# Kernel optimization log

Measured on AMD Instinct MI355X. Metric: run time of the kernel, lower is better.

Reference implementation:

```python
import jax, jax.numpy as jnp
import numpy as np

B, S, D, H = 2, 2048, 1024, 16
DK = D // H


def setup_inputs() -> dict:
    key = jax.random.key(0)
    ks = jax.random.split(key, 12)
    sc = 1.0 / np.sqrt(D)
    return {
        "q": jax.random.normal(ks[0], (B, S, D), jnp.float32),
        "k": jax.random.normal(ks[1], (B, S, D), jnp.float32),
        "v": jax.random.normal(ks[2], (B, S, D), jnp.float32),
        "mask": jax.random.randint(ks[3], (B, S), 0, 2, jnp.int32),
        "Wq": jax.random.normal(ks[4], (D, D), jnp.float32) * sc,
        "bq": jnp.zeros((D,), jnp.float32),
        "Wk": jax.random.normal(ks[5], (D, D), jnp.float32) * sc,
        "bk": jnp.zeros((D,), jnp.float32),
        "Wv": jax.random.normal(ks[6], (D, D), jnp.float32) * sc,
        "bv": jnp.zeros((D,), jnp.float32),
        "Wo": jax.random.normal(ks[7], (D, D), jnp.float32) * sc,
        "bo": jnp.zeros((D,), jnp.float32),
    }


def reference(q, k, v, mask, Wq, bq, Wk, bk, Wv, bv, Wo, bo):
    # Projections (flax nn.Dense: x @ W + b)
    query = q @ Wq + bq          # [B,S,D]
    key_ = k @ Wk + bk
    value = v @ Wv + bv
    # split heads -> [B,H,S,DK]
    def split(x):
        return x.reshape(B, S, H, DK).transpose(0, 2, 1, 3)
    qh, kh, vh = split(query), split(key_), split(value)
    scores = jnp.einsum('bhqd,bhkd->bhqk', qh, kh) / jnp.sqrt(jnp.float32(DK))
    # Faithful to source: mask=(mask==0); where(mask==0, -1e10, scores)
    # i.e. positions where ORIGINAL mask != 0 are set to -1e10.
    m = (mask == 0)[:, None, None, :]          # [B,1,1,S] bool
    scores = jnp.where(~m, jnp.float32(-1e10), scores)
    attn = jax.nn.softmax(scores, axis=-1)     # dropout deterministic (eval)
    x = jnp.einsum('bhqk,bhkd->bhqd', attn, vh)
    x = x.transpose(0, 2, 1, 3).reshape(B, S, D)
    return x @ Wo + bo
```

## Files before the change

### kernel.cpp

```cpp
#include <hip/hip_runtime.h>
#include <hip/hip_bf16.h>

typedef unsigned short u16;
typedef unsigned int u32;
typedef __attribute__((ext_vector_type(8))) __bf16 bf16x8;
typedef __attribute__((ext_vector_type(4))) float f32x4;
typedef __attribute__((ext_vector_type(16))) float f32x16;

constexpr int Bz = 2, Sq = 2048, Dm = 1024, Hn = 16, DK = 64;

__device__ __forceinline__ u16 f2bf(float f) {
    u32 u = __builtin_bit_cast(u32, f);
    return (u16)((u + 0x7FFFu + ((u >> 16) & 1u)) >> 16);
}

__device__ __forceinline__ u32 pack_bf16(float a, float b) {
#if __has_builtin(__builtin_amdgcn_cvt_pk_bf16_f32)
    return __builtin_bit_cast(u32, __builtin_amdgcn_cvt_pk_bf16_f32(a, b));
#else
    return (u32)f2bf(a) | ((u32)f2bf(b) << 16);
#endif
}

__device__ __forceinline__ bf16x8 lds_frag(const u16* p) {
    return __builtin_bit_cast(bf16x8, *(const uint4*)p);
}
__device__ __forceinline__ bf16x8 gfrag(const u16* p) {
    return __builtin_bit_cast(bf16x8, *(const uint4*)p);
}
__device__ __forceinline__ int swz(int r) { return (r ^ (r >> 3)) & 7; }

__device__ __forceinline__ void gll16(const u16* g, u16* l) {
    __builtin_amdgcn_global_load_lds(
        (const __attribute__((address_space(1))) void*)g,
        (__attribute__((address_space(3))) void*)l, 16, 0, 0);
}

__global__ __launch_bounds__(256) void mha_prep(
    const float* __restrict__ q, const float* __restrict__ k,
    const float* __restrict__ v,
    const float* __restrict__ w0, const float* __restrict__ w1,
    const float* __restrict__ w2, const float* __restrict__ w3,
    const int* __restrict__ mask,
    u16* __restrict__ qkv_dst, u16* __restrict__ wt_dst,
    float* __restrict__ biasg, int* __restrict__ compg, int* __restrict__ nkg)
{
    __shared__ float tl[64 * 65];
    __shared__ int sc[256];
    const int z = blockIdx.z, tid = threadIdx.x;
    if (z < 3) {
        const float* s = (z == 0) ? q : (z == 1) ? k : v;
        u16* d = qkv_dst + (size_t)z * 4 * 1024 * 1024;
        size_t i = ((size_t)blockIdx.x * 256 + tid) * 8;
        float4 a = *(const float4*)(s + i);
        float4 b = *(const float4*)(s + i + 4);
        *(uint4*)(d + i) = make_uint4(pack_bf16(a.x, a.y), pack_bf16(a.z, a.w),
                                      pack_bf16(b.x, b.y), pack_bf16(b.z, b.w));
        return;
    }
    const int bx = blockIdx.x;
    if (bx >= 1026) return;
    if (bx >= 1024) {
        const int b = bx - 1024;
        const int* mp = mask + b * Sq;
        int4 m0_ = ((const int4*)mp)[tid * 2];
        int4 m1_ = ((const int4*)mp)[tid * 2 + 1];
        int a[8];
        a[0] = (m0_.x == 0); a[1] = (m0_.y == 0); a[2] = (m0_.z == 0); a[3] = (m0_.w == 0);
        a[4] = (m1_.x == 0); a[5] = (m1_.y == 0); a[6] = (m1_.z == 0); a[7] = (m1_.w == 0);
        int cnt = 0;
#pragma unroll
        for (int j = 0; j < 8; j++) cnt += a[j];
        sc[tid] = cnt;
        __syncthreads();
        for (int off = 1; off < 256; off <<= 1) {
            int u = (tid >= off) ? sc[tid - off] : 0;
            int vv = sc[tid];
            __syncthreads();
            sc[tid] = vv + u;
            __syncthreads();
        }
        const int incl = sc[tid];
        const int nk = sc[255];
        int pa = incl - cnt;
        int pi = nk + tid * 8 - pa;
        int* cp = compg + b * Sq;
        float* bbp = biasg + b * Sq;
#pragma unroll
        for (int j = 0; j < 8; j++) {
            int pos = a[j] ? pa++ : pi++;
            cp[tid * 8 + j] = pos;
            bbp[pos] = a[j] ? 0.f : -1.44269504e10f;
        }
        if (tid == 0) nkg[b] = nk;
        return;
    }
    const int zi = bx >> 8, t = bx & 255, tr = t >> 4, tc = t & 15;
    const float* src = (zi == 0) ? w0 : (zi == 1) ? w1 : (zi == 2) ? w2 : w3;
    u16* d = wt_dst + (size_t)zi * Dm * Dm;
    {
        int r = tid >> 2, cq = (tid & 3) * 16;
        const float* sp = src + (size_t)(tr * 64 + r) * Dm + tc * 64 + cq;
#pragma unroll
        for (int j = 0; j < 4; j++) {
            float4 vv = *(const float4*)(sp + j * 4);
            tl[r * 65 + cq + j * 4 + 0] = vv.x;
            tl[r * 65 + cq + j * 4 + 1] = vv.y;
            tl[r * 65 + cq + j * 4 + 2] = vv.z;
            tl[r * 65 + cq + j * 4 + 3] = vv.w;
        }
    }
    __syncthreads();
    {
        int rr = tid >> 2, cc = (tid & 3) * 16;
        u16* dp = d + (size_t)(tc * 64 + rr) * Dm + tr * 64 + cc;
        u32 px[8];
#pragma unroll
        for (int j = 0; j < 8; j++)
            px[j] = pack_bf16(tl[(cc + 2 * j) * 65 + rr], tl[(cc + 2 * j + 1) * 65 + rr]);
        *(uint4*)dp       = make_uint4(px[0], px[1], px[2], px[3]);
        *(uint4*)(dp + 8) = make_uint4(px[4], px[5], px[6], px[7]);
    }
}

__device__ __forceinline__ void gemm_core_128128(
    const u16* __restrict__ Ab, const u16* __restrict__ Bb,
    u16* As, u16* Bs, f32x4 (&acc)[4][4])
{
    const int tid = threadIdx.x, lane = tid & 63;
    const int wm = (tid >> 7) & 1, wn = (tid >> 6) & 1;
    const int frow = lane & 15, quad = lane >> 4;

#pragma unroll
    for (int mi = 0; mi < 4; mi++)
#pragma unroll
        for (int ni = 0; ni < 4; ni++) acc[mi][ni] = (f32x4){0.f, 0.f, 0.f, 0.f};

    for (int k0 = 0; k0 < 1024; k0 += 64) {
#pragma unroll
        for (int i = 0; i < 4; i++) {
            int id = tid + i * 256, r = id >> 3, c = id & 7;
            gll16(Ab + (size_t)r * 1024 + k0 + (c ^ swz(r)) * 8, As + (size_t)id * 8);
        }
#pragma unroll
        for (int i = 0; i < 4; i++) {
            int id = tid + i * 256, r = id >> 3, c = id & 7;
            gll16(Bb + (size_t)r * 1024 + k0 + (c ^ swz(r)) * 8, Bs + (size_t)id * 8);
        }
        __syncthreads();
#pragma unroll
        for (int ks = 0; ks < 2; ks++) {
            bf16x8 af[4], bfr[4];
#pragma unroll
            for (int mi = 0; mi < 4; mi++) {
                int r = wm * 64 + mi * 16 + frow;
                af[mi] = lds_frag(As + r * 64 + ((ks * 4 + quad) ^ swz(r)) * 8);
            }
#pragma unroll
            for (int ni = 0; ni < 4; ni++) {
                int r = wn * 64 + ni * 16 + frow;
                bfr[ni] = lds_frag(Bs + r * 64 + ((ks * 4 + quad) ^ swz(r)) * 8);
            }
#pragma unroll
            for (int mi = 0; mi < 4; mi++)
#pragma unroll
                for (int ni = 0; ni < 4; ni++)
                    acc[mi][ni] = __builtin_amdgcn_mfma_f32_16x16x32_bf16(
                        af[mi], bfr[ni], acc[mi][ni], 0, 0, 0);
        }
        __syncthreads();
    }
}

__device__ __forceinline__ void gemm_core_12864(
    const u16* __restrict__ Ab, const u16* __restrict__ Bb,
    u16* As, u16* Bs, f32x4 (&acc)[4][2])
{
    const int tid = threadIdx.x, lane = tid & 63;
    const int wm = (tid >> 7) & 1, wn = (tid >> 6) & 1;
    const int frow = lane & 15, quad = lane >> 4;

#pragma unroll
    for (int mi = 0; mi < 4; mi++)
#pragma unroll
        for (int ni = 0; ni < 2; ni++) acc[mi][ni] = (f32x4){0.f, 0.f, 0.f, 0.f};

    for (int k0 = 0; k0 < 1024; k0 += 64) {
#pragma unroll
        for (int i = 0; i < 4; i++) {
            int id = tid + i * 256, r = id >> 3, c = id & 7;
            gll16(Ab + (size_t)r * 1024 + k0 + (c ^ swz(r)) * 8, As + (size_t)id * 8);
        }
#pragma unroll
        for (int i = 0; i < 2; i++) {
            int id = tid + i * 256, r = id >> 3, c = id & 7;
            gll16(Bb + (size_t)r * 1024 + k0 + (c ^ swz(r)) * 8, Bs + (size_t)id * 8);
        }
        __syncthreads();
#pragma unroll
        for (int ks = 0; ks < 2; ks++) {
            bf16x8 af[4], bfr[2];
#pragma unroll
            for (int mi = 0; mi < 4; mi++) {
                int r = wm * 64 + mi * 16 + frow;
                af[mi] = lds_frag(As + r * 64 + ((ks * 4 + quad) ^ swz(r)) * 8);
            }
#pragma unroll
            for (int ni = 0; ni < 2; ni++) {
                int r = wn * 32 + ni * 16 + frow;
                bfr[ni] = lds_frag(Bs + r * 64 + ((ks * 4 + quad) ^ swz(r)) * 8);
            }
#pragma unroll
            for (int mi = 0; mi < 4; mi++)
#pragma unroll
                for (int ni = 0; ni < 2; ni++)
                    acc[mi][ni] = __builtin_amdgcn_mfma_f32_16x16x32_bf16(
                        af[mi], bfr[ni], acc[mi][ni], 0, 0, 0);
        }
        __syncthreads();
    }
}

__global__ __launch_bounds__(256, 3) void mha_proj_qkv(
    const u16* __restrict__ Qb, const u16* __restrict__ Kb, const u16* __restrict__ Vb,
    const u16* __restrict__ Wqt, const u16* __restrict__ Wkt, const u16* __restrict__ Wvt,
    const float* __restrict__ bq, const float* __restrict__ bk, const float* __restrict__ bv,
    const int* __restrict__ comp,
    u16* __restrict__ Qh, u16* __restrict__ Kh, u16* __restrict__ Vt)
{
    __shared__ __align__(16) u16 As[128 * 64];
    __shared__ __align__(16) u16 Bs[128 * 64];
    const int z = blockIdx.z, bx = blockIdx.x;
    const u16* Ab; const u16* Bb; const float* bias;
    int m0, n0;
    if (z < 2) {
        m0 = (bx & 31) * 128;
        n0 = (bx >> 5) * 128;
        Ab = ((z == 0) ? Qb : Kb) + (size_t)m0 * Dm;
        Bb = ((z == 0) ? Wqt : Wkt) + (size_t)n0 * Dm;
        bias = (z == 0) ? bq : bk;
    } else {
        m0 = (bx >> 5) * 128;
        n0 = (bx & 31) * 128;
        Ab = Wvt + (size_t)m0 * Dm;
        Bb = Vb + (size_t)n0 * Dm;
        bias = bv;
    }

    f32x4 acc[4][4];
    gemm_core_128128(Ab, Bb, As, Bs, acc);

    const int tid = threadIdx.x, lane = tid & 63;
    const int wm = (tid >> 7) & 1, wn = (tid >> 6) & 1;
    const int frow = lane & 15, quad = lane >> 4;
    u16* dstq = (z == 0) ? Qh : Kh;
#pragma unroll
    for (int mi = 0; mi < 4; mi++)
#pragma unroll
        for (int ni = 0; ni < 4; ni++)
#pragma unroll
            for (int r = 0; r < 4; r++) {
                int i = m0 + wm * 64 + mi * 16 + quad * 4 + r;
                int j = n0 + wn * 64 + ni * 16 + frow;
                if (z < 2) {
                    float val = acc[mi][ni][r] + bias[j];
                    int b = i >> 11, s = i & (Sq - 1);
                    int h = j >> 6, dk = j & (DK - 1);
                    int srow = (z == 1) ? comp[b * Sq + s] : s;
                    dstq[((size_t)(b * Hn + h) * Sq + srow) * DK + dk] = f2bf(val);
                } else {
                    float val = acc[mi][ni][r] + bias[i];
                    int h = i >> 6, dk = i & (DK - 1);
                    int bj = j >> 11, s = j & (Sq - 1);
                    int cs = comp[bj * Sq + s];
                    int sp = (cs & ~12) | ((cs & 4) << 1) | ((cs & 8) >> 1);
                    Vt[((size_t)(bj * Hn + h) * DK + dk) * Sq + sp] = f2bf(val);
                }
            }
}

__global__ __launch_bounds__(512, 4) void mha_attn(
    const u16* __restrict__ Qh, const u16* __restrict__ Kh, const u16* __restrict__ Vt,
    const float* __restrict__ biasg, const int* __restrict__ nkg,
    u16* __restrict__ X)
{
    const int bh = blockIdx.x;
    const int b = bh >> 4;
    const int q0 = blockIdx.y * 64;
    const int tid = threadIdx.x, lane = tid & 63, w = tid >> 6;
    const int wq = w & 1, p = w >> 1;
    const int qc = lane & 31, half = lane >> 5;
    constexpr float C2 = 0.125f * 1.44269504f;

    __shared__ __align__(16) u16 SB[128 * 64 + 64 * 128];
    __shared__ float lsl[256];
    u16* Ks = SB;
    u16* Vs = SB + 128 * 64;

    const u16* Qp = Qh + (size_t)bh * Sq * DK;
    const u16* Kp = Kh + (size_t)bh * Sq * DK;
    const u16* Vp = Vt + (size_t)bh * DK * Sq;
    const float* bp = biasg + b * Sq;
    const int nk = nkg[b];
    const int nt = (nk + 127) >> 7;

    bf16x8 qf[4];
    {
        const u16* qrow = Qp + (size_t)(q0 + wq * 32 + qc) * DK + half * 8;
#pragma unroll
        for (int kc = 0; kc < 4; kc++) qf[kc] = gfrag(qrow + kc * 16);
    }

    const int idA = tid, idB = tid + 512;
    const u16* ksA = Kp + (size_t)(idA >> 3) * DK + ((idA & 7) ^ swz(idA >> 3)) * 8;
    const u16* ksB = Kp + (size_t)(idB >> 3) * DK + ((idB & 7) ^ swz(idB >> 3)) * 8;
    const u16* vsA = Vp + (size_t)(idA >> 4) * Sq + (((idA & 15) ^ ((idA >> 4) & 15)) * 8);
    const u16* vsB = Vp + (size_t)(idB >> 4) * Sq + (((idB & 15) ^ ((idB >> 4) & 15)) * 8);
    u16* kdA = Ks + idA * 8;
    u16* kdB = Ks + idB * 8;
    u16* vdA = Vs + idA * 8;
    u16* vdB = Vs + idB * 8;

    auto stage = [&](int kb) {
        gll16(ksA + (size_t)kb * DK, kdA);
        gll16(ksB + (size_t)kb * DK, kdB);
        gll16(vsA + kb, vdA);
        gll16(vsB + kb, vdB);
    };

    const int kr = p * 32 + qc;
    int kfo[4];
#pragma unroll
    for (int kc = 0; kc < 4; kc++)
        kfo[kc] = kr * 64 + (((kc * 2 + half) ^ swz(kr)) * 8);
    int vfo0[2], vfo1[2];
#pragma unroll
    for (int kc = 0; kc < 2; kc++) {
        int ch = p * 4 + kc * 2 + half;
        vfo0[kc] = qc * 128 + ((ch ^ (qc & 15)) * 8);
        vfo1[kc] = (32 + qc) * 128 + ((ch ^ (qc & 15)) * 8);
    }
    const float* bpw = bp + p * 32 + 4 * half;

    float l_l = 0.f;
    f32x16 o0, o1;
#pragma unroll
    for (int i = 0; i < 16; i++) { o0[i] = 0.f; o1[i] = 0.f; }

    for (int it = 0; it < nt; it++) {
        stage(it * 128);
        __syncthreads();

        f32x16 sT;
#pragma unroll
        for (int i = 0; i < 16; i++) sT[i] = 0.f;
        __builtin_amdgcn_s_setprio(1);
#pragma unroll
        for (int kc = 0; kc < 4; kc++) {
            bf16x8 ka = lds_frag(Ks + kfo[kc]);
            sT = __builtin_amdgcn_mfma_f32_32x32x16_bf16(ka, qf[kc], sT, 0, 0, 0);
        }
        __builtin_amdgcn_s_setprio(0);

        const int kb = it * 128;
        float t[16], rs = 0.f;
#pragma unroll
        for (int g = 0; g < 4; g++) {
            float4 mb = *(const float4*)(bpw + kb + 8 * g);
#pragma unroll
            for (int r = 0; r < 4; r++) {
                float bb = (r == 0) ? mb.x : (r == 1) ? mb.y : (r == 2) ? mb.z : mb.w;
                float a = __builtin_amdgcn_exp2f(fmaf(sT[g * 4 + r], C2, bb));
                t[g * 4 + r] = a; rs += a;
            }
        }
        l_l += rs;

        u32 pk[8];
#pragma unroll
        for (int i = 0; i < 8; i++) pk[i] = pack_bf16(t[2 * i], t[2 * i + 1]);

        __builtin_amdgcn_s_setprio(1);
#pragma unroll
        for (int kc = 0; kc < 2; kc++) {
            bf16x8 pf = __builtin_bit_cast(bf16x8,
                make_uint4(pk[4 * kc], pk[4 * kc + 1], pk[4 * kc + 2], pk[4 * kc + 3]));
            bf16x8 va0 = lds_frag(Vs + vfo0[kc]);
            bf16x8 va1 = lds_frag(Vs + vfo1[kc]);
            o0 = __builtin_amdgcn_mfma_f32_32x32x16_bf16(va0, pf, o0, 0, 0, 0);
            o1 = __builtin_amdgcn_mfma_f32_32x32x16_bf16(va1, pf, o1, 0, 0, 0);
        }
        __builtin_amdgcn_s_setprio(0);
        __syncthreads();
    }

    l_l += __shfl_xor(l_l, 32);
    float* fcb = (float*)SB;
    if (p >= 2) {
        float* fc = fcb + (size_t)(wq * 2 + (p & 1)) * 2048;
#pragma unroll
        for (int r = 0; r < 16; r++) fc[r * 64 + lane] = o0[r];
#pragma unroll
        for (int r = 0; r < 16; r++) fc[(16 + r) * 64 + lane] = o1[r];
        lsl[(wq * 2 + (p & 1)) * 64 + lane] = l_l;
    }
    __syncthreads();
    if (p < 2) {
        float* fc = fcb + (size_t)(wq * 2 + p) * 2048;
#pragma unroll
        for (int r = 0; r < 16; r++) o0[r] += fc[r * 64 + lane];
#pragma unroll
        for (int r = 0; r < 16; r++) o1[r] += fc[(16 + r) * 64 + lane];
        l_l += lsl[(wq * 2 + p) * 64 + lane];
    }
    if (p == 1) {
        float* fc = fcb + (size_t)(wq * 2 + 1) * 2048;
#pragma unroll
        for (int r = 0; r < 16; r++) fc[r * 64 + lane] = o0[r];
#pragma unroll
        for (int r = 0; r < 16; r++) fc[(16 + r) * 64 + lane] = o1[r];
        lsl[(wq * 2 + 1) * 64 + lane] = l_l;
    }
    __syncthreads();
    if (p == 0) {
        float* fc = fcb + (size_t)(wq * 2 + 1) * 2048;
#pragma unroll
        for (int r = 0; r < 16; r++) o0[r] += fc[r * 64 + lane];
#pragma unroll
        for (int r = 0; r < 16; r++) o1[r] += fc[(16 + r) * 64 + lane];
        l_l += lsl[(wq * 2 + 1) * 64 + lane];
        float inv = 1.0f / l_l;
        const int qg = q0 + wq * 32 + qc;
        u16* Xp = X + (size_t)(b * Sq + qg) * Dm + (bh & 15) * DK;
#pragma unroll
        for (int g = 0; g < 4; g++) {
            *(uint2*)&Xp[8 * g + 4 * half] =
                make_uint2(pack_bf16(o0[g * 4 + 0] * inv, o0[g * 4 + 1] * inv),
                           pack_bf16(o0[g * 4 + 2] * inv, o0[g * 4 + 3] * inv));
            *(uint2*)&Xp[32 + 8 * g + 4 * half] =
                make_uint2(pack_bf16(o1[g * 4 + 0] * inv, o1[g * 4 + 1] * inv),
                           pack_bf16(o1[g * 4 + 2] * inv, o1[g * 4 + 3] * inv));
        }
    }
}

__global__ __launch_bounds__(256) void mha_oproj(
    const u16* __restrict__ X, const u16* __restrict__ Wot,
    const float* __restrict__ bo, float* __restrict__ out)
{
    __shared__ __align__(16) u16 As[128 * 64];
    __shared__ __align__(16) u16 Bs[64 * 64];
    const int bx = blockIdx.x;
    const int m0 = (bx & 31) * 128, n0 = (bx >> 5) * 64;
    f32x4 acc[4][2];
    gemm_core_12864(X + (size_t)m0 * Dm, Wot + (size_t)n0 * Dm, As, Bs, acc);
    const int tid = threadIdx.x, lane = tid & 63;
    const int wm = (tid >> 7) & 1, wn = (tid >> 6) & 1;
    const int frow = lane & 15, quad = lane >> 4;
#pragma unroll
    for (int mi = 0; mi < 4; mi++)
#pragma unroll
        for (int ni = 0; ni < 2; ni++)
#pragma unroll
            for (int r = 0; r < 4; r++) {
                int m = m0 + wm * 64 + mi * 16 + quad * 4 + r;
                int n = n0 + wn * 32 + ni * 16 + frow;
                out[(size_t)m * Dm + n] = acc[mi][ni][r] + bo[n];
            }
}

extern "C" void kernel_launch(void* const* d_in, const int* in_sizes, int n_in,
                              void* d_out, int out_size, void* d_ws, size_t ws_size,
                              hipStream_t stream)
{
    const float* qin  = (const float*)d_in[0];
    const float* kin  = (const float*)d_in[1];
    const float* vin  = (const float*)d_in[2];
    const int*   mask = (const int*)d_in[3];
    const float* Wq   = (const float*)d_in[4];
    const float* bq   = (const float*)d_in[5];
    const float* Wk   = (const float*)d_in[6];
    const float* bk   = (const float*)d_in[7];
    const float* Wv   = (const float*)d_in[8];
    const float* bv   = (const float*)d_in[9];
    const float* Wo   = (const float*)d_in[10];
    const float* bo   = (const float*)d_in[11];
    float* out = (float*)d_out;

    u16* ws = (u16*)d_ws;
    const size_t MW = (size_t)Dm * Dm;
    const size_t MT = (size_t)Bz * Sq * Dm;
    u16* Wqt = ws;
    u16* Wkt = ws + MW;
    u16* Wvt = ws + 2 * MW;
    u16* Wot = ws + 3 * MW;
    u16* Qb  = ws + 4 * MW;
    u16* Kb  = Qb + MT;
    u16* Vb  = Kb + MT;
    u16* Qh  = Vb + MT;
    u16* Kh  = Qh + MT;
    u16* Vt  = Kh + MT;
    float* biasg = (float*)(Vt + MT);
    int*   compg = (int*)(biasg + Bz * Sq);
    int*   nkg   = (int*)(compg + Bz * Sq);
    u16* X   = Qb;

    hipLaunchKernelGGL(mha_prep, dim3(2048, 1, 4), dim3(256), 0, stream,
                       qin, kin, vin, Wq, Wk, Wv, Wo, mask, Qb, Wqt, biasg, compg, nkg);
    hipLaunchKernelGGL(mha_proj_qkv, dim3(256, 1, 3), dim3(256), 0, stream,
                       Qb, Kb, Vb, Wqt, Wkt, Wvt, bq, bk, bv, compg, Qh, Kh, Vt);
    hipLaunchKernelGGL(mha_attn, dim3(32, 32), dim3(512), 0, stream,
                       Qh, Kh, Vt, biasg, nkg, X);
    hipLaunchKernelGGL(mha_oproj, dim3(512), dim3(256), 0, stream,
                       X, Wot, bo, out);
}
```

Baseline: 226.0 us.

## Double attention query tile per block, halving key-split waves

Each attention block now covers 128 queries with 4 query waves and 2 key-split partitions, instead of 64 queries with 2 query waves and 4 partitions. Each wave processes two 32-key sub-tiles per 128-key stage, so every staged K/V tile in LDS serves twice as many queries. The cross-wave reduction shrinks to a single merge step. The grid is halved, which means fewer blocks, less parallelism and more registers used per wave.

Result: slower. 245.0 us (+8.4%).

```diff
diff --git a/kernel.cpp b/kernel.cpp
--- a/kernel.cpp
+++ b/kernel.cpp
@@ -286,9 +286,9 @@
 {
     const int bh = blockIdx.x;
     const int b = bh >> 4;
-    const int q0 = blockIdx.y * 64;
+    const int q0 = blockIdx.y * 128;
     const int tid = threadIdx.x, lane = tid & 63, w = tid >> 6;
-    const int wq = w & 1, p = w >> 1;
+    const int wq = w & 3, p = w >> 2;
     const int qc = lane & 31, half = lane >> 5;
     constexpr float C2 = 0.125f * 1.44269504f;
 
@@ -328,19 +328,7 @@
         gll16(vsB + kb, vdB);
     };
 
-    const int kr = p * 32 + qc;
-    int kfo[4];
-#pragma unroll
-    for (int kc = 0; kc < 4; kc++)
-        kfo[kc] = kr * 64 + (((kc * 2 + half) ^ swz(kr)) * 8);
-    int vfo0[2], vfo1[2];
-#pragma unroll
-    for (int kc = 0; kc < 2; kc++) {
-        int ch = p * 4 + kc * 2 + half;
-        vfo0[kc] = qc * 128 + ((ch ^ (qc & 15)) * 8);
-        vfo1[kc] = (32 + qc) * 128 + ((ch ^ (qc & 15)) * 8);
-    }
-    const float* bpw = bp + p * 32 + 4 * half;
+    const float* bpw = bp + p * 64 + 4 * half;
 
     float l_l = 0.f;
     f32x16 o0, o1;
@@ -350,85 +338,73 @@
     for (int it = 0; it < nt; it++) {
         stage(it * 128);
         __syncthreads();
-
-        f32x16 sT;
-#pragma unroll
-        for (int i = 0; i < 16; i++) sT[i] = 0.f;
-        __builtin_amdgcn_s_setprio(1);
-#pragma unroll
-        for (int kc = 0; kc < 4; kc++) {
-            bf16x8 ka = lds_frag(Ks + kfo[kc]);
-            sT = __builtin_amdgcn_mfma_f32_32x32x16_bf16(ka, qf[kc], sT, 0, 0, 0);
-        }
-        __builtin_amdgcn_s_setprio(0);
-
         const int kb = it * 128;
-        float t[16], rs = 0.f;
-#pragma unroll
-        for (int g = 0; g < 4; g++) {
-            float4 mb = *(const float4*)(bpw + kb + 8 * g);
-#pragma unroll
-            for (int r = 0; r < 4; r++) {
-                float bb = (r == 0) ? mb.x : (r == 1) ? mb.y : (r == 2) ? mb.z : mb.w;
-                float a = __builtin_amdgcn_exp2f(fmaf(sT[g * 4 + r], C2, bb));
-                t[g * 4 + r] = a; rs += a;
-            }
-        }
-        l_l += rs;
-
-        u32 pk[8];
-#pragma unroll
-        for (int i = 0; i < 8; i++) pk[i] = pack_bf16(t[2 * i], t[2 * i + 1]);
-
-        __builtin_amdgcn_s_setprio(1);
-#pragma unroll
-        for (int kc = 0; kc < 2; kc++) {
-            bf16x8 pf = __builtin_bit_cast(bf16x8,
-                make_uint4(pk[4 * kc], pk[4 * kc + 1], pk[4 * kc + 2], pk[4 * kc + 3]));
-            bf16x8 va0 = lds_frag(Vs + vfo0[kc]);
-            bf16x8 va1 = lds_frag(Vs + vfo1[kc]);
-            o0 = __builtin_amdgcn_mfma_f32_32x32x16_bf16(va0, pf, o0, 0, 0, 0);
-            o1 = __builtin_amdgcn_mfma_f32_32x32x16_bf16(va1, pf, o1, 0, 0, 0);
-        }
-        __builtin_amdgcn_s_setprio(0);
+
+#pragma unroll
+        for (int s = 0; s < 2; s++) {
+            const int kr = p * 64 + s * 32 + qc;
+            f32x16 sT;
+#pragma unroll
+            for (int i = 0; i < 16; i++) sT[i] = 0.f;
+            __builtin_amdgcn_s_setprio(1);
+#pragma unroll
+            for (int kc = 0; kc < 4; kc++) {
+                bf16x8 ka = lds_frag(Ks + kr * 64 + (((kc * 2 + half) ^ swz(kr)) * 8));
+                sT = __builtin_amdgcn_mfma_f32_32x32x16_bf16(ka, qf[kc], sT, 0, 0, 0);
+            }
+            __builtin_amdgcn_s_setprio(0);
+
+            float t[16], rs = 0.f;
+#pragma unroll
+            for (int g = 0; g < 4; g++) {
+                float4 mb = *(const float4*)(bpw + kb + s * 32 + 8 * g);
+#pragma unroll
+                for (int r = 0; r < 4; r++) {
+                    float bb = (r == 0) ? mb.x : (r == 1) ? mb.y : (r == 2) ? mb.z : mb.w;
+                    float a = __builtin_amdgcn_exp2f(fmaf(sT[g * 4 + r], C2, bb));
+                    t[g * 4 + r] = a; rs += a;
+                }
+            }
+            l_l += rs;
+
+            u32 pk[8];
+#pragma unroll
+            for (int i = 0; i < 8; i++) pk[i] = pack_bf16(t[2 * i], t[2 * i + 1]);
+
+            __builtin_amdgcn_s_setprio(1);
+#pragma unroll
+            for (int kc = 0; kc < 2; kc++) {
+                bf16x8 pf = __builtin_bit_cast(bf16x8,
+                    make_uint4(pk[4 * kc], pk[4 * kc + 1], pk[4 * kc + 2], pk[4 * kc + 3]));
+                int ch = p * 8 + s * 4 + kc * 2 + half;
+                bf16x8 va0 = lds_frag(Vs + qc * 128 + ((ch ^ (qc & 15)) * 8));
+                bf16x8 va1 = lds_frag(Vs + (32 + qc) * 128 + ((ch ^ (qc & 15)) * 8));
+                o0 = __builtin_amdgcn_mfma_f32_32x32x16_bf16(va0, pf, o0, 0, 0, 0);
+                o1 = __builtin_amdgcn_mfma_f32_32x32x16_bf16(va1, pf, o1, 0, 0, 0);
+            }
+            __builtin_amdgcn_s_setprio(0);
+        }
         __syncthreads();
     }
 
     l_l += __shfl_xor(l_l, 32);
     float* fcb = (float*)SB;
-    if (p >= 2) {
-        float* fc = fcb + (size_t)(wq * 2 + (p & 1)) * 2048;
+    if (p == 1) {
+        float* fc = fcb + (size_t)wq * 2048;
 #pragma unroll
         for (int r = 0; r < 16; r++) fc[r * 64 + lane] = o0[r];
 #pragma unroll
         for (int r = 0; r < 16; r++) fc[(16 + r) * 64 + lane] = o1[r];
-        lsl[(wq * 2 + (p & 1)) * 64 + lane] = l_l;
-    }
-    __syncthreads();
-    if (p < 2) {
-        float* fc = fcb + (size_t)(wq * 2 + p) * 2048;
-#pragma unroll
-        for (int r = 0; r < 16; r++) o0[r] += fc[r * 64 + lane];
-#pragma unroll
-        for (int r = 0; r < 16; r++) o1[r] += fc[(16 + r) * 64 + lane];
-        l_l += lsl[(wq * 2 + p) * 64 + lane];
-    }
-    if (p == 1) {
-        float* fc = fcb + (size_t)(wq * 2 + 1) * 2048;
-#pragma unroll
-        for (int r = 0; r < 16; r++) fc[r * 64 + lane] = o0[r];
-#pragma unroll
-        for (int r = 0; r < 16; r++) fc[(16 + r) * 64 + lane] = o1[r];
-        lsl[(wq * 2 + 1) * 64 + lane] = l_l;
+        lsl[wq * 64 + lane] = l_l;
     }
     __syncthreads();
     if (p == 0) {
-        float* fc = fcb + (size_t)(wq * 2 + 1) * 2048;
+        float* fc = fcb + (size_t)wq * 2048;
 #pragma unroll
         for (int r = 0; r < 16; r++) o0[r] += fc[r * 64 + lane];
 #pragma unroll
         for (int r = 0; r < 16; r++) o1[r] += fc[(16 + r) * 64 + lane];
-        l_l += lsl[(wq * 2 + 1) * 64 + lane];
+        l_l += lsl[wq * 64 + lane];
         float inv = 1.0f / l_l;
         const int qg = q0 + wq * 32 + qc;
         u16* Xp = X + (size_t)(b * Sq + qg) * Dm + (bh & 15) * DK;
@@ -509,7 +485,7 @@
                        qin, kin, vin, Wq, Wk, Wv, Wo, mask, Qb, Wqt, biasg, compg, nkg);
     hipLaunchKernelGGL(mha_proj_qkv, dim3(256, 1, 3), dim3(256), 0, stream,
                        Qb, Kb, Vb, Wqt, Wkt, Wvt, bq, bk, bv, compg, Qh, Kh, Vt);
-    hipLaunchKernelGGL(mha_attn, dim3(32, 32), dim3(512), 0, stream,
+    hipLaunchKernelGGL(mha_attn, dim3(32, 16), dim3(512), 0, stream,
                        Qh, Kh, Vt, biasg, nkg, X);
     hipLaunchKernelGGL(mha_oproj, dim3(512), dim3(256), 0, stream,
                        X, Wot, bo, out);
```
